# Kernel optimization log

Measured on AMD Instinct MI355X. Metric: run time of the kernel, lower is better.

The kernel has to match this reference:

```python
import jax, jax.numpy as jnp
import numpy as np
from jax import lax

EPS = 1e-5

def _sign(x):
    # sign with sign(0)=+1, as used in XNOR-style binarization
    return jnp.where(x >= 0, 1.0, -1.0).astype(x.dtype)

def binarize(x):
    # straight-through estimator: forward = sign(x), backward = identity
    return x + lax.stop_gradient(_sign(x) - x)

def batchnorm(x, p):
    # p: [4, C] rows = (gamma, beta, running_mean, running_var); eval-mode BN
    g, b, m, v = p[0], p[1], p[2], p[3]
    shape = (1, -1) + (1,) * (x.ndim - 2)
    inv = g / jnp.sqrt(v + EPS)
    return (x - m.reshape(shape)) * inv.reshape(shape) + b.reshape(shape)

def conv2d(x, w):
    return lax.conv_general_dilated(x, w, window_strides=(1, 1), padding='VALID',
                                    dimension_numbers=('NCHW', 'OIHW', 'NCHW'))

def maxpool2(x):
    return lax.reduce_window(x, -jnp.inf, lax.max, (1, 1, 2, 2), (1, 1, 2, 2), 'VALID')

def hardtanh(x):
    return jnp.clip(x, -1.0, 1.0)


def setup_inputs() -> dict:
    key = jax.random.key(0)
    ks = jax.random.split(key, 16)
    B = 16384
    x = jax.random.normal(ks[0], (B, 3, 22, 22), jnp.float32)
    w1 = jax.random.normal(ks[1], (32, 3, 3, 3), jnp.float32) * 0.1
    w2 = jax.random.normal(ks[2], (32, 32, 3, 3), jnp.float32) * 0.1
    w3 = jax.random.normal(ks[3], (64, 32, 3, 3), jnp.float32) * 0.1
    w_fc1 = jax.random.normal(ks[4], (128, 64), jnp.float32) * 0.1
    w_fc2 = jax.random.normal(ks[5], (2, 128), jnp.float32) * 0.1
    w_fc3 = jax.random.normal(ks[6], (4, 128), jnp.float32) * 0.1

    def make_bn(k, c):
        k1, k2, k3, k4 = jax.random.split(k, 4)
        gamma = jax.random.uniform(k1, (c,), jnp.float32, 0.5, 1.5)
        beta = jax.random.normal(k2, (c,), jnp.float32) * 0.1
        mean = jax.random.normal(k3, (c,), jnp.float32) * 0.1
        var = jax.random.uniform(k4, (c,), jnp.float32, 0.5, 1.5)
        return jnp.stack([gamma, beta, mean, var])  # [4, C]

    bn1 = make_bn(ks[7], 32)
    bn2 = make_bn(ks[8], 32)
    bn3 = make_bn(ks[9], 64)
    bn4 = make_bn(ks[10], 128)
    bn5 = make_bn(ks[11], 2)
    bn6 = make_bn(ks[12], 4)
    return {'x': x, 'w1': w1, 'w2': w2, 'w3': w3, 'w_fc1': w_fc1, 'w_fc2': w_fc2,
            'w_fc3': w_fc3, 'bn1': bn1, 'bn2': bn2, 'bn3': bn3, 'bn4': bn4,
            'bn5': bn5, 'bn6': bn6}


def reference(x, w1, w2, w3, w_fc1, w_fc2, w_fc3, bn1, bn2, bn3, bn4, bn5, bn6):
    # binary=True, binarize_input=True, bitwidth=input_bitwidth=1:
    # every BinarizeConv2d/BinarizeLinear binarizes both its input and weights.
    h = hardtanh(batchnorm(conv2d(binarize(x), binarize(w1)), bn1))   # [B,32,20,20]
    h = maxpool2(h)                                                    # [B,32,10,10]
    h = hardtanh(batchnorm(conv2d(binarize(h), binarize(w2)), bn2))   # [B,32,8,8]
    h = maxpool2(h)                                                    # [B,32,4,4]
    h = hardtanh(batchnorm(conv2d(binarize(h), binarize(w3)), bn3))   # [B,64,2,2]
    h = maxpool2(h)                                                    # [B,64,1,1]
    h = h.reshape(-1, 64)                                              # [B,64]
    h = hardtanh(batchnorm(binarize(h) @ binarize(w_fc1).T, bn4))      # [B,128]
    out1 = jax.nn.softmax(batchnorm(h @ w_fc2.T, bn5), axis=1)         # [B,2]
    out2 = batchnorm(h @ w_fc3.T, bn6)                                 # [B,4]
    return (out1, out2)
```

## Files before the change

kernel.cpp:

```cpp
#include <hip/hip_runtime.h>
#include <cstdint>
#include <cmath>

typedef int  v4i  __attribute__((ext_vector_type(4)));
typedef int  v16i __attribute__((ext_vector_type(16)));
typedef unsigned int u32x4 __attribute__((ext_vector_type(4)));

#define OFF_W1   0
#define OFF_T1   32
#define OFF_W3   384
#define OFF_T3   960
#define OFF_WFC1 1024
#define OFF_A4   1280
#define OFF_C4   1408
#define OFF_WF2  1536
#define OFF_WF3  1792
#define OFF_BN5  2304
#define OFF_BN6  2308
#define OFF_B2   2560
#define OFF_T2C  4864

__device__ __forceinline__ int thr_neg(double nterms, double g, double b, double m, double v) {
    double inv = g / sqrt(v + 1e-5);
    double t = m - b / inv;
    double thr = floor((nterms - t) * 0.5);
    if (thr < -2147000000.0) thr = -2147000000.0;
    if (thr >  2147000000.0) thr =  2147000000.0;
    return -((int)thr + 1);
}

__device__ __forceinline__ int thr_c_neg(double g, double b, double m, double v) {
    double inv = g / sqrt(v + 1e-5);
    double t = m - b / inv;
    double ct = ceil(t);
    if (ct < -2147000000.0) ct = -2147000000.0;
    if (ct >  2147000000.0) ct =  2147000000.0;
    return -(int)ct;
}

__global__ void k_prep(const float* __restrict__ w1, const float* __restrict__ w2,
                       const float* __restrict__ w3, const float* __restrict__ wfc1,
                       const float* __restrict__ wfc2, const float* __restrict__ wfc3,
                       const float* __restrict__ bn1, const float* __restrict__ bn2,
                       const float* __restrict__ bn3, const float* __restrict__ bn4,
                       const float* __restrict__ bn5, const float* __restrict__ bn6,
                       unsigned int* __restrict__ ws) {
    __shared__ float stage[9216];
    int t = threadIdx.x;
    int blk = blockIdx.x;
    float* wsf = (float*)ws;
    int*   wsi = (int*)ws;

    if (blk == 0) {
        for (int i = t; i < 864; i += 256) stage[i] = w1[i];
        __syncthreads();
        if (t < 32) {
            unsigned int bits = 0;
            for (int j = 0; j < 27; ++j) bits |= (stage[t*27+j] >= 0.f ? 1u : 0u) << j;
            ws[OFF_W1 + t] = bits;
            wsi[OFF_T1 + t]  = thr_neg(27.0, bn1[t], bn1[32+t], bn1[64+t], bn1[96+t]);
            wsi[OFF_T2C + t] = thr_c_neg(bn2[t], bn2[32+t], bn2[64+t], bn2[96+t]);
        }
        for (int i = t; i < 256; i += 256) wsf[OFF_WF2 + i] = wfc2[i];
        for (int i = t; i < 512; i += 256) wsf[OFF_WF3 + i] = wfc3[i];
        if (t < 2) {
            float g = bn5[t], b = bn5[2+t], m = bn5[4+t], v = bn5[6+t];
            float inv = g / sqrtf(v + 1e-5f);
            wsf[OFF_BN5 + t]     = inv;
            wsf[OFF_BN5 + 2 + t] = b - m * inv;
        }
        if (t >= 4 && t < 8) {
            int j = t - 4;
            float g = bn6[j], b = bn6[4+j], m = bn6[8+j], v = bn6[12+j];
            float inv = g / sqrtf(v + 1e-5f);
            wsf[OFF_BN6 + j]     = inv;
            wsf[OFF_BN6 + 4 + j] = b - m * inv;
        }
    } else if (blk == 1) {
        for (int i = t; i < 9216; i += 256) stage[i] = w2[i];
        __syncthreads();
        for (int idx = t; idx < 2304; idx += 256) {
            int s   = idx >> 8;
            int rem = idx & 255;
            int l   = rem >> 2;
            int reg = rem & 3;
            int och = l & 31;
            int icb = ((l >> 5) << 4) + (reg << 2);
            unsigned int wv = 0;
            #pragma unroll
            for (int j = 0; j < 4; ++j) {
                int ic = icb + j;
                unsigned int by = (stage[(och*32 + ic)*9 + s] >= 0.f) ? 0x01u : 0xFFu;
                wv |= by << (8*j);
            }
            ws[OFF_B2 + idx] = wv;
        }
    } else if (blk == 2 || blk == 3) {
        int base = (blk - 2) * 9216;
        for (int i = t; i < 9216; i += 256) stage[i] = w3[base + i];
        __syncthreads();
        for (int idx = t; idx < 288; idx += 256) {
            int o = idx / 9, k = idx - o*9;
            unsigned int bits = 0;
            for (int i = 0; i < 32; ++i)
                bits |= (stage[(o*32+i)*9 + k] >= 0.f ? 1u : 0u) << i;
            ws[OFF_W3 + base/32 + idx] = bits;
        }
    } else {
        for (int i = t; i < 8192; i += 256) stage[i] = wfc1[i];
        __syncthreads();
        if (t < 128) {
            unsigned int lo = 0, hi = 0;
            for (int j = 0; j < 32; ++j) lo |= (stage[t*64+j]    >= 0.f ? 1u : 0u) << j;
            for (int j = 0; j < 32; ++j) hi |= (stage[t*64+32+j] >= 0.f ? 1u : 0u) << j;
            ws[OFF_WFC1 + 2*t]     = lo;
            ws[OFF_WFC1 + 2*t + 1] = hi;
            float g = bn4[t], b = bn4[128+t], m = bn4[256+t], v = bn4[384+t];
            float inv = g / sqrtf(v + 1e-5f);
            wsf[OFF_A4 + t] = -2.f * inv;
            wsf[OFF_C4 + t] = (64.f - m) * inv + b;
        }
        if (t >= 128 && t < 192) {
            int j = t - 128;
            wsi[OFF_T3 + j] = thr_neg(288.0, bn3[j], bn3[64+j], bn3[128+j], bn3[192+j]);
        }
    }
}

#define WSTRIDE 900
__global__ __launch_bounds__(256, 4) void k_main(const float* __restrict__ x,
                                                 const unsigned int* __restrict__ ws,
                                                 float* __restrict__ out, int B) {
    __shared__ __align__(16) unsigned int s_u[4 * WSTRIDE];

    const int tid = threadIdx.x & 63;
    const int wid = threadIdx.x >> 6;
    const int b   = blockIdx.x * 4 + wid;
    if (b >= B) return;
    const float* wsf = (const float*)ws;
    const int*   wsi = (const int*)ws;

    unsigned int* bytes = s_u + wid * WSTRIDE;
    unsigned int* inrow = bytes;
    unsigned int* c1    = bytes + 66;
    unsigned int* pb1   = bytes + 800;

    for (int r = tid; r < 66; r += 64) {
        int c = r / 22, y = r - c*22;
        const float2* p = (const float2*)(x + ((size_t)b*3 + c)*484 + (size_t)y*22);
        unsigned int bits = 0;
        #pragma unroll
        for (int j = 0; j < 11; ++j) {
            float2 v = p[j];
            bits |= (v.x >= 0.f ? 1u : 0u) << (2*j);
            bits |= (v.y >= 0.f ? 1u : 0u) << (2*j+1);
        }
        inrow[r] = bits;
    }
    __builtin_amdgcn_wave_barrier();

    v4i Breg[9];
    {
        const v4i* __restrict__ Bfr = (const v4i*)(ws + OFF_B2);
        #pragma unroll
        for (int s = 0; s < 9; ++s) Breg[s] = Bfr[s*64 + tid];
    }
    const int nthr2 = wsi[OFF_T2C + (tid & 31)];

    for (int pos = tid; pos < 400; pos += 64) {
        int y = pos / 20, xx = pos - y*20;
        unsigned int g = 0;
        #pragma unroll
        for (int c = 0; c < 3; ++c)
            #pragma unroll
            for (int dy = 0; dy < 3; ++dy)
                g |= ((inrow[c*22 + y + dy] >> xx) & 7u) << (c*9 + dy*3);
        unsigned int word = 0;
        #pragma unroll
        for (int o = 31; o >= 0; --o) {
            unsigned int s = (unsigned int)(__popc(g ^ ws[OFF_W1 + o]) + wsi[OFF_T1 + o]);
            word = __builtin_amdgcn_alignbit(word, s, 31);
        }
        c1[pos] = word;
    }
    __builtin_amdgcn_wave_barrier();

    for (int p = tid; p < 100; p += 64) {
        int py = p / 10, px = p - py*10;
        int base = (2*py)*20 + 2*px;
        pb1[p] = c1[base] | c1[base+1] | c1[base+20] | c1[base+21];
    }
    __builtin_amdgcn_wave_barrier();

    #pragma unroll
    for (int i = 0; i < 4; ++i) {
        int c2 = tid + 64*i;
        if (c2 < 200) {
            int hi  = (c2 >= 100) ? 1 : 0;
            int pos = c2 - hi*100;
            unsigned int w = pb1[pos];
            int sh = hi << 4;
            u32x4 o;
            #pragma unroll
            for (int j = 0; j < 4; ++j) {
                unsigned int nib = (w >> (sh + 4*j)) & 0xFu;
                unsigned int sp  = (nib * 0x204081u) & 0x01010101u;
                o[j] = __builtin_amdgcn_perm(0u, 0x000001FFu, sp);
            }
            *(u32x4*)(bytes + c2*4) = o;
        }
    }
    __builtin_amdgcn_wave_barrier();

    unsigned int w3r[9];
    #pragma unroll
    for (int k = 0; k < 9; ++k) w3r[k] = ws[OFF_W3 + tid*9 + k];
    const int negt3 = wsi[OFF_T3 + tid];

    unsigned int pb2w[16];
    {
        const int hi = tid >> 5;
        #pragma unroll
        for (int tile = 0; tile < 2; ++tile) {
            int r   = tid & 31;
            int gq  = tile*8 + (r >> 2);
            int sub = r & 3;
            int y   = ((gq >> 2) << 1) + (sub >> 1);
            int x   = ((gq & 3) << 1) + (sub & 1);
            const v4i* __restrict__ Ab = (const v4i*)(bytes + (hi*100 + y*10 + x)*4);
            v16i acc;
            #pragma unroll
            for (int j = 0; j < 16; ++j) acc[j] = nthr2;
            __builtin_amdgcn_s_setprio(1);
            #pragma unroll
            for (int s = 0; s < 9; ++s) {
                int dy = s / 3, dx = s - dy*3;
                v4i a = Ab[dy*10 + dx];
                acc = __builtin_amdgcn_mfma_i32_32x32x32_i8(a, Breg[s], acc, 0, 0, 0);
            }
            __builtin_amdgcn_s_setprio(0);
            #pragma unroll
            for (int g = 0; g < 4; ++g) {
                int m0 = acc[4*g]   > acc[4*g+1] ? acc[4*g]   : acc[4*g+1];
                int m1 = acc[4*g+2] > acc[4*g+3] ? acc[4*g+2] : acc[4*g+3];
                int mx = m0 > m1 ? m0 : m1;
                unsigned long long bal = __ballot(mx >= 0);
                pb2w[tile*8 + 2*g]     = (unsigned int)bal;
                pb2w[tile*8 + 2*g + 1] = (unsigned int)(bal >> 32);
            }
        }
    }

    unsigned long long b3 = 0;
    {
        unsigned int oracc = 0;
        #pragma unroll
        for (int py = 0; py < 2; ++py)
            #pragma unroll
            for (int px = 0; px < 2; ++px) {
                int s = negt3;
                #pragma unroll
                for (int dy = 0; dy < 3; ++dy)
                    #pragma unroll
                    for (int dx = 0; dx < 3; ++dx)
                        s += __popc(pb2w[(py+dy)*4 + px + dx] ^ w3r[dy*3+dx]);
                oracc |= (unsigned int)s;
            }
        b3 = __ballot((int)oracc < 0);
    }

    float h0, h1;
    {
        const unsigned long long* wfc1b = (const unsigned long long*)(ws + OFF_WFC1);
        int pc0 = __popcll(b3 ^ wfc1b[tid]);
        int pc1 = __popcll(b3 ^ wfc1b[tid + 64]);
        float p0 = fmaf((float)pc0, wsf[OFF_A4 + tid],      wsf[OFF_C4 + tid]);
        float p1 = fmaf((float)pc1, wsf[OFF_A4 + tid + 64], wsf[OFF_C4 + tid + 64]);
        h0 = fminf(1.f, fmaxf(-1.f, p0));
        h1 = fminf(1.f, fmaxf(-1.f, p1));
    }

    {
        float part[6];
        #pragma unroll
        for (int j = 0; j < 2; ++j)
            part[j] = h0 * wsf[OFF_WF2 + j*128 + tid] + h1 * wsf[OFF_WF2 + j*128 + 64 + tid];
        #pragma unroll
        for (int j = 0; j < 4; ++j)
            part[2+j] = h0 * wsf[OFF_WF3 + j*128 + tid] + h1 * wsf[OFF_WF3 + j*128 + 64 + tid];
        #pragma unroll
        for (int off = 32; off; off >>= 1) {
            #pragma unroll
            for (int j = 0; j < 6; ++j)
                part[j] += __shfl_xor(part[j], off);
        }
        if (tid < 6) {
            if (tid < 2) {
                float y0 = part[0]*wsf[OFF_BN5+0] + wsf[OFF_BN5+2];
                float y1 = part[1]*wsf[OFF_BN5+1] + wsf[OFF_BN5+3];
                float mx = fmaxf(y0, y1);
                float e0 = expf(y0 - mx), e1 = expf(y1 - mx);
                float r  = 1.f / (e0 + e1);
                out[(size_t)b*2 + tid] = (tid == 0 ? e0 : e1) * r;
            } else {
                int j = tid - 2;
                out[(size_t)B*2 + (size_t)b*4 + j] = part[2+j]*wsf[OFF_BN6+j] + wsf[OFF_BN6+4+j];
            }
        }
    }
}

extern "C" void kernel_launch(void* const* d_in, const int* in_sizes, int n_in,
                              void* d_out, int out_size, void* d_ws, size_t ws_size,
                              hipStream_t stream) {
    const float* x    = (const float*)d_in[0];
    const float* w1   = (const float*)d_in[1];
    const float* w2   = (const float*)d_in[2];
    const float* w3   = (const float*)d_in[3];
    const float* wfc1 = (const float*)d_in[4];
    const float* wfc2 = (const float*)d_in[5];
    const float* wfc3 = (const float*)d_in[6];
    const float* bn1  = (const float*)d_in[7];
    const float* bn2  = (const float*)d_in[8];
    const float* bn3  = (const float*)d_in[9];
    const float* bn4  = (const float*)d_in[10];
    const float* bn5  = (const float*)d_in[11];
    const float* bn6  = (const float*)d_in[12];
    unsigned int* ws  = (unsigned int*)d_ws;
    float* out        = (float*)d_out;
    int B = in_sizes[0] / 1452;

    k_prep<<<5, 256, 0, stream>>>(w1, w2, w3, wfc1, wfc2, wfc3,
                                  bn1, bn2, bn3, bn4, bn5, bn6, ws);
    k_main<<<(B + 3) / 4, 256, 0, stream>>>(x, ws, out, B);
}
```

Before: 179.9 us.

## Process two images per wavefront to amortize weight loads and expose ILP

Each wavefront now handles two batch images instead of one. The MFMA B fragments, w3 weights, thresholds and FC weights are loaded once and reused for both, and the two independent dependency chains are interleaved to give more instruction-level parallelism. The grid is halved and LDS per block doubles to 8*WSTRIDE words. Input binarization now builds the sign bits with alignbit on the float sign bit and a final inversion. The costs are higher register pressure and LDS use, which may lower occupancy under launch_bounds(256,4). The sign trick also changes the result for -0.0, which the reference maps to +1 but this code maps to -1.

After: 184.2 us. 2.4% more time.

```diff
diff --git a/kernel.cpp b/kernel.cpp
--- a/kernel.cpp
+++ b/kernel.cpp
@@ -131,31 +131,52 @@
 __global__ __launch_bounds__(256, 4) void k_main(const float* __restrict__ x,
                                                  const unsigned int* __restrict__ ws,
                                                  float* __restrict__ out, int B) {
-    __shared__ __align__(16) unsigned int s_u[4 * WSTRIDE];
+    __shared__ __align__(16) unsigned int s_u[8 * WSTRIDE];
 
     const int tid = threadIdx.x & 63;
     const int wid = threadIdx.x >> 6;
-    const int b   = blockIdx.x * 4 + wid;
-    if (b >= B) return;
+    const int b0  = blockIdx.x * 8 + wid * 2;
+    const int b1  = b0 + 1;
+    if (b0 >= B) return;
+    const bool has1 = (b1 < B);
     const float* wsf = (const float*)ws;
     const int*   wsi = (const int*)ws;
 
-    unsigned int* bytes = s_u + wid * WSTRIDE;
-    unsigned int* inrow = bytes;
-    unsigned int* c1    = bytes + 66;
-    unsigned int* pb1   = bytes + 800;
+    unsigned int* baseA = s_u + wid * (2 * WSTRIDE);
+    unsigned int* baseB = baseA + WSTRIDE;
+    unsigned int* inA   = baseA;
+    unsigned int* inB   = baseB;
+    unsigned int* c1A   = baseA + 66;
+    unsigned int* c1B   = baseB + 66;
+    unsigned int* pb1A  = baseA + 800;
+    unsigned int* pb1B  = baseB + 800;
+    unsigned int* bytA  = baseA;
+    unsigned int* bytB  = baseB;
 
     for (int r = tid; r < 66; r += 64) {
         int c = r / 22, y = r - c*22;
-        const float2* p = (const float2*)(x + ((size_t)b*3 + c)*484 + (size_t)y*22);
-        unsigned int bits = 0;
-        #pragma unroll
-        for (int j = 0; j < 11; ++j) {
-            float2 v = p[j];
-            bits |= (v.x >= 0.f ? 1u : 0u) << (2*j);
-            bits |= (v.y >= 0.f ? 1u : 0u) << (2*j+1);
-        }
-        inrow[r] = bits;
+        {
+            const float2* p = (const float2*)(x + ((size_t)b0*3 + c)*484 + (size_t)y*22);
+            unsigned int w = 0;
+            #pragma unroll
+            for (int j = 10; j >= 0; --j) {
+                float2 v = p[j];
+                w = __builtin_amdgcn_alignbit(w, __float_as_uint(v.y), 31);
+                w = __builtin_amdgcn_alignbit(w, __float_as_uint(v.x), 31);
+            }
+            inA[r] = ~w;
+        }
+        if (has1) {
+            const float2* p = (const float2*)(x + ((size_t)b1*3 + c)*484 + (size_t)y*22);
+            unsigned int w = 0;
+            #pragma unroll
+            for (int j = 10; j >= 0; --j) {
+                float2 v = p[j];
+                w = __builtin_amdgcn_alignbit(w, __float_as_uint(v.y), 31);
+                w = __builtin_amdgcn_alignbit(w, __float_as_uint(v.x), 31);
+            }
+            inB[r] = ~w;
+        }
     }
     __builtin_amdgcn_wave_barrier();
 
@@ -169,26 +190,33 @@
 
     for (int pos = tid; pos < 400; pos += 64) {
         int y = pos / 20, xx = pos - y*20;
-        unsigned int g = 0;
+        unsigned int gA = 0, gB = 0;
         #pragma unroll
         for (int c = 0; c < 3; ++c)
             #pragma unroll
-            for (int dy = 0; dy < 3; ++dy)
-                g |= ((inrow[c*22 + y + dy] >> xx) & 7u) << (c*9 + dy*3);
-        unsigned int word = 0;
+            for (int dy = 0; dy < 3; ++dy) {
+                int ri = c*22 + y + dy, sh = c*9 + dy*3;
+                gA |= ((inA[ri] >> xx) & 7u) << sh;
+                gB |= ((inB[ri] >> xx) & 7u) << sh;
+            }
+        unsigned int wA = 0, wB = 0;
         #pragma unroll
         for (int o = 31; o >= 0; --o) {
-            unsigned int s = (unsigned int)(__popc(g ^ ws[OFF_W1 + o]) + wsi[OFF_T1 + o]);
-            word = __builtin_amdgcn_alignbit(word, s, 31);
-        }
-        c1[pos] = word;
+            unsigned int sA = (unsigned int)(__popc(gA ^ ws[OFF_W1 + o]) + wsi[OFF_T1 + o]);
+            unsigned int sB = (unsigned int)(__popc(gB ^ ws[OFF_W1 + o]) + wsi[OFF_T1 + o]);
+            wA = __builtin_amdgcn_alignbit(wA, sA, 31);
+            wB = __builtin_amdgcn_alignbit(wB, sB, 31);
+        }
+        c1A[pos] = wA;
+        c1B[pos] = wB;
     }
     __builtin_amdgcn_wave_barrier();
 
     for (int p = tid; p < 100; p += 64) {
         int py = p / 10, px = p - py*10;
         int base = (2*py)*20 + 2*px;
-        pb1[p] = c1[base] | c1[base+1] | c1[base+20] | c1[base+21];
+        pb1A[p] = c1A[base] | c1A[base+1] | c1A[base+20] | c1A[base+21];
+        pb1B[p] = c1B[base] | c1B[base+1] | c1B[base+20] | c1B[base+21];
     }
     __builtin_amdgcn_wave_barrier();
 
@@ -198,16 +226,18 @@
         if (c2 < 200) {
             int hi  = (c2 >= 100) ? 1 : 0;
             int pos = c2 - hi*100;
-            unsigned int w = pb1[pos];
-            int sh = hi << 4;
-            u32x4 o;
+            int sh  = hi << 4;
+            unsigned int wa = pb1A[pos], wb = pb1B[pos];
+            u32x4 oa, ob;
             #pragma unroll
             for (int j = 0; j < 4; ++j) {
-                unsigned int nib = (w >> (sh + 4*j)) & 0xFu;
-                unsigned int sp  = (nib * 0x204081u) & 0x01010101u;
-                o[j] = __builtin_amdgcn_perm(0u, 0x000001FFu, sp);
-            }
-            *(u32x4*)(bytes + c2*4) = o;
+                unsigned int na = (wa >> (sh + 4*j)) & 0xFu;
+                unsigned int nb = (wb >> (sh + 4*j)) & 0xFu;
+                oa[j] = __builtin_amdgcn_perm(0u, 0x000001FFu, (na * 0x204081u) & 0x01010101u);
+                ob[j] = __builtin_amdgcn_perm(0u, 0x000001FFu, (nb * 0x204081u) & 0x01010101u);
+            }
+            *(u32x4*)(bytA + c2*4) = oa;
+            *(u32x4*)(bytB + c2*4) = ob;
         }
     }
     __builtin_amdgcn_wave_barrier();
@@ -217,17 +247,20 @@
     for (int k = 0; k < 9; ++k) w3r[k] = ws[OFF_W3 + tid*9 + k];
     const int negt3 = wsi[OFF_T3 + tid];
 
-    unsigned int pb2w[16];
+    unsigned int pb2wA[16], pb2wB[16];
     {
         const int hi = tid >> 5;
-        #pragma unroll
-        for (int tile = 0; tile < 2; ++tile) {
-            int r   = tid & 31;
+        const int r   = tid & 31;
+        #pragma unroll
+        for (int half = 0; half < 4; ++half) {
+            int tile = half & 1;
+            const unsigned int* byt = (half < 2) ? bytA : bytB;
+            unsigned int* pb2w      = (half < 2) ? pb2wA : pb2wB;
             int gq  = tile*8 + (r >> 2);
             int sub = r & 3;
             int y   = ((gq >> 2) << 1) + (sub >> 1);
             int x   = ((gq & 3) << 1) + (sub & 1);
-            const v4i* __restrict__ Ab = (const v4i*)(bytes + (hi*100 + y*10 + x)*4);
+            const v4i* __restrict__ Ab = (const v4i*)(byt + (hi*100 + y*10 + x)*4);
             v16i acc;
             #pragma unroll
             for (int j = 0; j < 16; ++j) acc[j] = nthr2;
@@ -251,47 +284,62 @@
         }
     }
 
-    unsigned long long b3 = 0;
-    {
-        unsigned int oracc = 0;
+    unsigned long long b3A, b3B;
+    {
+        unsigned int orA = 0, orB = 0;
         #pragma unroll
         for (int py = 0; py < 2; ++py)
             #pragma unroll
             for (int px = 0; px < 2; ++px) {
-                int s = negt3;
+                int sA = negt3, sB = negt3;
                 #pragma unroll
                 for (int dy = 0; dy < 3; ++dy)
                     #pragma unroll
-                    for (int dx = 0; dx < 3; ++dx)
-                        s += __popc(pb2w[(py+dy)*4 + px + dx] ^ w3r[dy*3+dx]);
-                oracc |= (unsigned int)s;
-            }
-        b3 = __ballot((int)oracc < 0);
-    }
-
-    float h0, h1;
+                    for (int dx = 0; dx < 3; ++dx) {
+                        sA += __popc(pb2wA[(py+dy)*4 + px + dx] ^ w3r[dy*3+dx]);
+                        sB += __popc(pb2wB[(py+dy)*4 + px + dx] ^ w3r[dy*3+dx]);
+                    }
+                orA |= (unsigned int)sA;
+                orB |= (unsigned int)sB;
+            }
+        b3A = __ballot((int)orA < 0);
+        b3B = __ballot((int)orB < 0);
+    }
+
+    float h0A, h1A, h0B, h1B;
     {
         const unsigned long long* wfc1b = (const unsigned long long*)(ws + OFF_WFC1);
-        int pc0 = __popcll(b3 ^ wfc1b[tid]);
-        int pc1 = __popcll(b3 ^ wfc1b[tid + 64]);
-        float p0 = fmaf((float)pc0, wsf[OFF_A4 + tid],      wsf[OFF_C4 + tid]);
-        float p1 = fmaf((float)pc1, wsf[OFF_A4 + tid + 64], wsf[OFF_C4 + tid + 64]);
-        h0 = fminf(1.f, fmaxf(-1.f, p0));
-        h1 = fminf(1.f, fmaxf(-1.f, p1));
-    }
-
-    {
-        float part[6];
-        #pragma unroll
-        for (int j = 0; j < 2; ++j)
-            part[j] = h0 * wsf[OFF_WF2 + j*128 + tid] + h1 * wsf[OFF_WF2 + j*128 + 64 + tid];
-        #pragma unroll
-        for (int j = 0; j < 4; ++j)
-            part[2+j] = h0 * wsf[OFF_WF3 + j*128 + tid] + h1 * wsf[OFF_WF3 + j*128 + 64 + tid];
+        unsigned long long wlo = wfc1b[tid], whi = wfc1b[tid + 64];
+        float a4l = wsf[OFF_A4 + tid],      c4l = wsf[OFF_C4 + tid];
+        float a4h = wsf[OFF_A4 + tid + 64], c4h = wsf[OFF_C4 + tid + 64];
+        float p0A = fmaf((float)__popcll(b3A ^ wlo), a4l, c4l);
+        float p1A = fmaf((float)__popcll(b3A ^ whi), a4h, c4h);
+        float p0B = fmaf((float)__popcll(b3B ^ wlo), a4l, c4l);
+        float p1B = fmaf((float)__popcll(b3B ^ whi), a4h, c4h);
+        h0A = fminf(1.f, fmaxf(-1.f, p0A));
+        h1A = fminf(1.f, fmaxf(-1.f, p1A));
+        h0B = fminf(1.f, fmaxf(-1.f, p0B));
+        h1B = fminf(1.f, fmaxf(-1.f, p1B));
+    }
+
+    {
+        float part[12];
+        #pragma unroll
+        for (int j = 0; j < 2; ++j) {
+            float wl = wsf[OFF_WF2 + j*128 + tid], wh = wsf[OFF_WF2 + j*128 + 64 + tid];
+            part[j]     = h0A * wl + h1A * wh;
+            part[6 + j] = h0B * wl + h1B * wh;
+        }
+        #pragma unroll
+        for (int j = 0; j < 4; ++j) {
+            float wl = wsf[OFF_WF3 + j*128 + tid], wh = wsf[OFF_WF3 + j*128 + 64 + tid];
+            part[2 + j]  = h0A * wl + h1A * wh;
+            part[8 + j]  = h0B * wl + h1B * wh;
+        }
         #pragma unroll
         for (int off = 32; off; off >>= 1) {
             #pragma unroll
-            for (int j = 0; j < 6; ++j)
+            for (int j = 0; j < 12; ++j)
                 part[j] += __shfl_xor(part[j], off);
         }
         if (tid < 6) {
@@ -300,11 +348,21 @@
                 float y1 = part[1]*wsf[OFF_BN5+1] + wsf[OFF_BN5+3];
                 float mx = fmaxf(y0, y1);
                 float e0 = expf(y0 - mx), e1 = expf(y1 - mx);
-                float r  = 1.f / (e0 + e1);
-                out[(size_t)b*2 + tid] = (tid == 0 ? e0 : e1) * r;
+                float rr = 1.f / (e0 + e1);
+                out[(size_t)b0*2 + tid] = (tid == 0 ? e0 : e1) * rr;
+                if (has1) {
+                    float z0 = part[6]*wsf[OFF_BN5+0] + wsf[OFF_BN5+2];
+                    float z1 = part[7]*wsf[OFF_BN5+1] + wsf[OFF_BN5+3];
+                    float mz = fmaxf(z0, z1);
+                    float f0 = expf(z0 - mz), f1 = expf(z1 - mz);
+                    float rz = 1.f / (f0 + f1);
+                    out[(size_t)b1*2 + tid] = (tid == 0 ? f0 : f1) * rz;
+                }
             } else {
                 int j = tid - 2;
-                out[(size_t)B*2 + (size_t)b*4 + j] = part[2+j]*wsf[OFF_BN6+j] + wsf[OFF_BN6+4+j];
+                out[(size_t)B*2 + (size_t)b0*4 + j] = part[2+j]*wsf[OFF_BN6+j] + wsf[OFF_BN6+4+j];
+                if (has1)
+                    out[(size_t)B*2 + (size_t)b1*4 + j] = part[8+j]*wsf[OFF_BN6+j] + wsf[OFF_BN6+4+j];
             }
         }
     }
@@ -332,5 +390,5 @@
 
     k_prep<<<5, 256, 0, stream>>>(w1, w2, w3, wfc1, wfc2, wfc3,
                                   bn1, bn2, bn3, bn4, bn5, bn6, ws);
-    k_main<<<(B + 3) / 4, 256, 0, stream>>>(x, ws, out, B);
-}
+    k_main<<<(B + 7) / 8, 256, 0, stream>>>(x, ws, out, B);
+}
```

## Launch one single-wave block per sample and simplify input sign packing

Applied to the files above, without the earlier changes.

Replaces the 4-wave blocks, each wave handling one sample in its own LDS slice, with 64-thread blocks that each process one sample using a 900-word LDS buffer. Input binarization now builds the sign mask with alignbit shifts of the float sign bits followed by an inversion, replacing per-element compares and ORs. The MFMA accumulator seed is hoisted out of the tile loop. The intent is better scheduling flexibility and less per-block coupling, at the cost of four times as many blocks and no launch-bounds occupancy hint.

After: 182.2 us. No clear change (+1.3%).

```diff
diff --git a/kernel.cpp b/kernel.cpp
--- a/kernel.cpp
+++ b/kernel.cpp
@@ -127,35 +127,33 @@
     }
 }
 
-#define WSTRIDE 900
-__global__ __launch_bounds__(256, 4) void k_main(const float* __restrict__ x,
-                                                 const unsigned int* __restrict__ ws,
-                                                 float* __restrict__ out, int B) {
-    __shared__ __align__(16) unsigned int s_u[4 * WSTRIDE];
-
-    const int tid = threadIdx.x & 63;
-    const int wid = threadIdx.x >> 6;
-    const int b   = blockIdx.x * 4 + wid;
+__global__ __launch_bounds__(64) void k_main(const float* __restrict__ x,
+                                             const unsigned int* __restrict__ ws,
+                                             float* __restrict__ out, int B) {
+    __shared__ __align__(16) unsigned int s_u[900];
+
+    const int tid = threadIdx.x;
+    const int b   = blockIdx.x;
     if (b >= B) return;
     const float* wsf = (const float*)ws;
     const int*   wsi = (const int*)ws;
 
-    unsigned int* bytes = s_u + wid * WSTRIDE;
-    unsigned int* inrow = bytes;
-    unsigned int* c1    = bytes + 66;
-    unsigned int* pb1   = bytes + 800;
+    unsigned int* bytes = s_u;
+    unsigned int* inrow = s_u;
+    unsigned int* c1    = s_u + 66;
+    unsigned int* pb1   = s_u + 800;
 
     for (int r = tid; r < 66; r += 64) {
         int c = r / 22, y = r - c*22;
         const float2* p = (const float2*)(x + ((size_t)b*3 + c)*484 + (size_t)y*22);
-        unsigned int bits = 0;
-        #pragma unroll
-        for (int j = 0; j < 11; ++j) {
+        unsigned int w = 0;
+        #pragma unroll
+        for (int j = 10; j >= 0; --j) {
             float2 v = p[j];
-            bits |= (v.x >= 0.f ? 1u : 0u) << (2*j);
-            bits |= (v.y >= 0.f ? 1u : 0u) << (2*j+1);
-        }
-        inrow[r] = bits;
+            w = __builtin_amdgcn_alignbit(w, __float_as_uint(v.y), 31);
+            w = __builtin_amdgcn_alignbit(w, __float_as_uint(v.x), 31);
+        }
+        inrow[r] = ~w;
     }
     __builtin_amdgcn_wave_barrier();
 
@@ -220,20 +218,21 @@
     unsigned int pb2w[16];
     {
         const int hi = tid >> 5;
+        const int r  = tid & 31;
+        v16i seed;
+        #pragma unroll
+        for (int j = 0; j < 16; ++j) seed[j] = nthr2;
         #pragma unroll
         for (int tile = 0; tile < 2; ++tile) {
-            int r   = tid & 31;
             int gq  = tile*8 + (r >> 2);
             int sub = r & 3;
             int y   = ((gq >> 2) << 1) + (sub >> 1);
             int x   = ((gq & 3) << 1) + (sub & 1);
             const v4i* __restrict__ Ab = (const v4i*)(bytes + (hi*100 + y*10 + x)*4);
-            v16i acc;
-            #pragma unroll
-            for (int j = 0; j < 16; ++j) acc[j] = nthr2;
             __builtin_amdgcn_s_setprio(1);
-            #pragma unroll
-            for (int s = 0; s < 9; ++s) {
+            v16i acc = __builtin_amdgcn_mfma_i32_32x32x32_i8(Ab[0], Breg[0], seed, 0, 0, 0);
+            #pragma unroll
+            for (int s = 1; s < 9; ++s) {
                 int dy = s / 3, dx = s - dy*3;
                 v4i a = Ab[dy*10 + dx];
                 acc = __builtin_amdgcn_mfma_i32_32x32x32_i8(a, Breg[s], acc, 0, 0, 0);
@@ -332,5 +331,5 @@
 
     k_prep<<<5, 256, 0, stream>>>(w1, w2, w3, wfc1, wfc2, wfc3,
                                   bn1, bn2, bn3, bn4, bn5, bn6, ws);
-    k_main<<<(B + 3) / 4, 256, 0, stream>>>(x, ws, out, B);
-}
+    k_main<<<B, 64, 0, stream>>>(x, ws, out, B);
+}
```
